# Optimization experiments

Measured on AMD Instinct MI355X. Metric: run time of the kernel, lower is better.

Reference implementation:

```python
import jax, jax.numpy as jnp
import numpy as np

H, DH = 4, 64          # heads, dim_head (match init_kwargs)
E = 128                # edge_dim
INNER = H * DH
NEG = -jnp.finfo(jnp.float32).max


def setup_inputs() -> dict:
    key = jax.random.key(0)
    ks = jax.random.split(key, 8)
    b, i, j = 1, 256, 256
    s = lambda fan_in: 1.0 / np.sqrt(fan_in)
    return {
        "inter_edges": jax.random.normal(ks[0], (b, i, j, E), jnp.float32),
        "ab_mask": jnp.ones((b, i), dtype=bool),
        "at_mask": jnp.ones((b, j), dtype=bool),
        "Wq": jax.random.normal(ks[1], (E, INNER), jnp.float32) * s(E),
        "Wk": jax.random.normal(ks[2], (E, INNER), jnp.float32) * s(E),
        "Wv": jax.random.normal(ks[3], (E, INNER), jnp.float32) * s(E),
        "Web": jax.random.normal(ks[4], (E, H), jnp.float32) * s(E),
        "Wg": jax.random.normal(ks[5], (E, INNER), jnp.float32) * s(E),
        "bg": jnp.zeros((INNER,), jnp.float32),
        "Wo": jax.random.normal(ks[6], (INNER, E), jnp.float32) * s(INNER),
        "bo": jnp.zeros((E,), jnp.float32),
    }


def reference(inter_edges, ab_mask, at_mask, Wq, Wk, Wv, Web, Wg, bg, Wo, bo):
    b, i, j, e = inter_edges.shape  # b must be 1 (bias broadcast in original)

    def split_hd(t):  # 'b i j (h d) -> (b h) i j d'
        return t.reshape(b, i, j, H, DH).transpose(0, 3, 1, 2, 4).reshape(b * H, i, j, DH)

    q = split_hd(inter_edges @ Wq)
    k = split_hd(inter_edges @ Wk)
    v = split_hd(inter_edges @ Wv)

    # to_ebias: [b,i,j,h].transpose(0,-1) -> [h,i,j,b]; broadcasts over key axis (b==1)
    z_bias = jnp.swapaxes(inter_edges @ Web, 0, -1)

    # gate uses (d h) split order, unlike q/k/v's (h d)
    gate = jax.nn.sigmoid(inter_edges @ Wg + bg)
    z_gate = gate.reshape(b, i, j, DH, H).transpose(0, 4, 1, 2, 3).reshape(b * H, i, j, DH)

    sim = jnp.einsum('hijd,hikd->hijk', q, k) * (DH ** -0.5) + z_bias

    mask = ab_mask[:, :, None] & at_mask[:, None, :]          # [b,i,j]
    mask = jnp.repeat(mask, H, axis=0)                        # [(b h),i,j]
    sim = jnp.where(mask[..., None], sim, NEG)                # mask whole (i,j) query rows

    attn = jax.nn.softmax(sim, axis=-1)
    # original einsum 'h i j k, h i j d -> h i j d' == v * attn.sum(-1)
    out = v * jnp.sum(attn, axis=-1, keepdims=True)
    out = z_gate * out
    out = out.reshape(b, H, i, j, DH).transpose(0, 2, 3, 1, 4).reshape(b, i, j, INNER)
    return out @ Wo + bo
```

## Files before the change

### kernel.cpp

```cpp
#include <hip/hip_runtime.h>

typedef __attribute__((ext_vector_type(8))) short short8;
typedef __attribute__((ext_vector_type(4))) float f32x4;

__device__ __forceinline__ unsigned short f2b(float x) {
  union { float f; unsigned u; } v; v.f = x;
  unsigned r = v.u + 0x7fffu + ((v.u >> 16) & 1u);
  return (unsigned short)(r >> 16);
}

__global__ __launch_bounds__(256) void prep_kernel(
    const float* __restrict__ Wv, const float* __restrict__ Wg,
    const float* __restrict__ bgv, const float* __restrict__ Wo,
    unsigned short* __restrict__ W1T, unsigned short* __restrict__ WoT,
    float* __restrict__ bg2)
{
  int t = blockIdx.x * 256 + threadIdx.x;
  if (t < 512 * 128) {
    int c = t >> 7, e = t & 127;
    float val;
    if (c < 256) {
      val = Wv[e * 256 + c];
    } else {
      int cc = c - 256;
      val = Wg[e * 256 + ((cc & 63) << 2) + (cc >> 6)];
    }
    W1T[t] = f2b(val);
  } else if (t < 512 * 128 + 128 * 256) {
    int u = t - 512 * 128;
    int o = u >> 8, c = u & 255;
    WoT[u] = f2b(Wo[c * 128 + o]);
  } else if (t < 512 * 128 + 128 * 256 + 256) {
    int c = t - (512 * 128 + 128 * 256);
    bg2[c] = bgv[((c & 63) << 2) + (c >> 6)];
  }
}

__global__ __launch_bounds__(256) void fused_kernel(
    const float* __restrict__ X,
    const unsigned short* __restrict__ W1T,
    const unsigned short* __restrict__ WoT,
    const float* __restrict__ bg2,
    const float* __restrict__ bo,
    float* __restrict__ Out)
{
  __shared__ unsigned short Xs[64 * 128];
  __shared__ unsigned short Ys[64 * 256];

  const int tid  = threadIdx.x;
  const int lane = tid & 63;
  const int wave = tid >> 6;
  const int l15  = lane & 15;
  const int lhi  = lane >> 4;
  const long rowbase = (long)blockIdx.x * 64;

  const float4* Xblk = reinterpret_cast<const float4*>(X + rowbase * 128);
  #pragma unroll
  for (int it = 0; it < 8; ++it) {
    int idx4 = it * 256 + tid;
    float4 f = Xblk[idx4];
    int e0  = idx4 * 4;
    int row = e0 >> 7;
    int col = e0 & 127;
    int sidx = (row * 128 + col) ^ ((row & 7) << 3);
    ushort4 u;
    u.x = f2b(f.x); u.y = f2b(f.y); u.z = f2b(f.z); u.w = f2b(f.w);
    *reinterpret_cast<ushort4*>(&Xs[sidx]) = u;
  }
  __syncthreads();

  short8 afrag[4][4];
  #pragma unroll
  for (int mt = 0; mt < 4; ++mt) {
    int row = mt * 16 + l15;
    #pragma unroll
    for (int ks = 0; ks < 4; ++ks) {
      int sidx = (row * 128 + ks * 32 + lhi * 8) ^ ((row & 7) << 3);
      afrag[mt][ks] = *reinterpret_cast<const short8*>(&Xs[sidx]);
    }
  }

  const f32x4 vzero = {0.f, 0.f, 0.f, 0.f};

  #pragma unroll
  for (int t = 0; t < 4; ++t) {
    int c0 = (wave * 4 + t) * 16;
    const unsigned short* WVrow = W1T + (c0 + l15) * 128 + lhi * 8;
    const unsigned short* WGrow = WVrow + 256 * 128;
    f32x4 accV[4], accG[4];
    #pragma unroll
    for (int mt = 0; mt < 4; ++mt) { accV[mt] = vzero; accG[mt] = vzero; }
    #pragma unroll
    for (int ks = 0; ks < 4; ++ks) {
      short8 bV = *reinterpret_cast<const short8*>(WVrow + ks * 32);
      short8 bG = *reinterpret_cast<const short8*>(WGrow + ks * 32);
      #pragma unroll
      for (int mt = 0; mt < 4; ++mt) {
        accV[mt] = __builtin_amdgcn_mfma_f32_16x16x32_bf16(afrag[mt][ks], bV, accV[mt], 0, 0, 0);
        accG[mt] = __builtin_amdgcn_mfma_f32_16x16x32_bf16(afrag[mt][ks], bG, accG[mt], 0, 0, 0);
      }
    }
    float bgval = bg2[c0 + l15];
    #pragma unroll
    for (int mt = 0; mt < 4; ++mt) {
      #pragma unroll
      for (int r = 0; r < 4; ++r) {
        int row = mt * 16 + lhi * 4 + r;
        float z = accG[mt][r] + bgval;
        float g = 1.0f / (1.0f + __expf(-z));
        float y = g * accV[mt][r];
        int sidx = (row * 256 + c0 + l15) ^ ((row & 7) << 3);
        Ys[sidx] = f2b(y);
      }
    }
  }
  __syncthreads();

  f32x4 acc2[2][4];
  #pragma unroll
  for (int nn = 0; nn < 2; ++nn)
    #pragma unroll
    for (int mt = 0; mt < 4; ++mt) acc2[nn][mt] = vzero;

  int o0 = wave * 16;
  #pragma unroll
  for (int ks = 0; ks < 8; ++ks) {
    short8 b0 = *reinterpret_cast<const short8*>(WoT + (o0 + l15) * 256 + ks * 32 + lhi * 8);
    short8 b1 = *reinterpret_cast<const short8*>(WoT + (64 + o0 + l15) * 256 + ks * 32 + lhi * 8);
    #pragma unroll
    for (int mt = 0; mt < 4; ++mt) {
      int row = mt * 16 + l15;
      int sidx = (row * 256 + ks * 32 + lhi * 8) ^ ((row & 7) << 3);
      short8 a = *reinterpret_cast<const short8*>(&Ys[sidx]);
      acc2[0][mt] = __builtin_amdgcn_mfma_f32_16x16x32_bf16(a, b0, acc2[0][mt], 0, 0, 0);
      acc2[1][mt] = __builtin_amdgcn_mfma_f32_16x16x32_bf16(a, b1, acc2[1][mt], 0, 0, 0);
    }
  }
  #pragma unroll
  for (int nn = 0; nn < 2; ++nn) {
    int o = nn * 64 + o0 + l15;
    float bov = bo[o];
    #pragma unroll
    for (int mt = 0; mt < 4; ++mt) {
      #pragma unroll
      for (int r = 0; r < 4; ++r) {
        long row = rowbase + mt * 16 + lhi * 4 + r;
        Out[row * 128 + o] = acc2[nn][mt][r] + bov;
      }
    }
  }
}

extern "C" void kernel_launch(void* const* d_in, const int* in_sizes, int n_in,
                              void* d_out, int out_size, void* d_ws, size_t ws_size,
                              hipStream_t stream) {
  const float* X   = (const float*)d_in[0];
  const float* Wv  = (const float*)d_in[5];
  const float* Wg  = (const float*)d_in[7];
  const float* bg  = (const float*)d_in[8];
  const float* Wo  = (const float*)d_in[9];
  const float* bo  = (const float*)d_in[10];

  unsigned short* W1T = (unsigned short*)d_ws;
  unsigned short* WoT = W1T + 512 * 128;
  float*          bg2 = (float*)(WoT + 128 * 256);

  prep_kernel<<<385, 256, 0, stream>>>(Wv, Wg, bg, Wo, W1T, WoT, bg2);

  float* Out = (float*)d_out;
  fused_kernel<<<1024, 256, 0, stream>>>(X, W1T, WoT, bg2, bo, Out);
}
```

Before: 126.3 us.

## Alias X and Y LDS buffers, raise occupancy hint, coalesce prep reads

The fused kernel now reuses a single shared-memory buffer for both the bf16 input tile and the gated intermediate, with an extra barrier after the A fragments are loaded into registers. This cuts LDS per block from 48KB to 32KB, and the launch bound now asks for 5 waves per SIMD so more blocks can be resident. The prep kernel is rewritten to read the weights in coalesced order and scatter the transposed writes. The tighter register budget could cause spills, and the extra barrier adds a sync.

```diff
diff --git a/kernel.cpp b/kernel.cpp
--- a/kernel.cpp
+++ b/kernel.cpp
@@ -16,27 +16,25 @@
     float* __restrict__ bg2)
 {
   int t = blockIdx.x * 256 + threadIdx.x;
-  if (t < 512 * 128) {
-    int c = t >> 7, e = t & 127;
-    float val;
-    if (c < 256) {
-      val = Wv[e * 256 + c];
-    } else {
-      int cc = c - 256;
-      val = Wg[e * 256 + ((cc & 63) << 2) + (cc >> 6)];
-    }
-    W1T[t] = f2b(val);
-  } else if (t < 512 * 128 + 128 * 256) {
-    int u = t - 512 * 128;
-    int o = u >> 8, c = u & 255;
-    WoT[u] = f2b(Wo[c * 128 + o]);
-  } else if (t < 512 * 128 + 128 * 256 + 256) {
-    int c = t - (512 * 128 + 128 * 256);
-    bg2[c] = bgv[((c & 63) << 2) + (c >> 6)];
+  if (t < 32768) {
+    int e = t >> 8, c = t & 255;
+    W1T[c * 128 + e] = f2b(Wv[t]);
+  } else if (t < 65536) {
+    int s = t - 32768;
+    int e = s >> 8, g = s & 255;
+    int cc = ((g & 3) << 6) + (g >> 2);
+    W1T[(256 + cc) * 128 + e] = f2b(Wg[s]);
+  } else if (t < 65536 + 32768) {
+    int s = t - 65536;
+    int c = s >> 7, o = s & 127;
+    WoT[o * 256 + c] = f2b(Wo[s]);
+  } else if (t < 65536 + 32768 + 256) {
+    int g = t - (65536 + 32768);
+    bg2[((g & 3) << 6) + (g >> 2)] = bgv[g];
   }
 }
 
-__global__ __launch_bounds__(256) void fused_kernel(
+__global__ __launch_bounds__(256, 5) void fused_kernel(
     const float* __restrict__ X,
     const unsigned short* __restrict__ W1T,
     const unsigned short* __restrict__ WoT,
@@ -44,8 +42,9 @@
     const float* __restrict__ bo,
     float* __restrict__ Out)
 {
-  __shared__ unsigned short Xs[64 * 128];
-  __shared__ unsigned short Ys[64 * 256];
+  __shared__ unsigned short smem[64 * 256];
+  unsigned short* Xs = smem;
+  unsigned short* Ys = smem;
 
   const int tid  = threadIdx.x;
   const int lane = tid & 63;
@@ -79,6 +78,7 @@
       afrag[mt][ks] = *reinterpret_cast<const short8*>(&Xs[sidx]);
     }
   }
+  __syncthreads();
 
   const f32x4 vzero = {0.f, 0.f, 0.f, 0.f};
 
@@ -165,7 +165,8 @@
   unsigned short* WoT = W1T + 512 * 128;
   float*          bg2 = (float*)(WoT + 128 * 256);
 
-  prep_kernel<<<385, 256, 0, stream>>>(Wv, Wg, bg, Wo, W1T, WoT, bg2);
+  prep_kernel<<<(65536 + 32768 + 256 + 255) / 256 + 1, 256, 0, stream>>>(
+      Wv, Wg, bg, Wo, W1T, WoT, bg2);
 
   float* Out = (float*)d_out;
   fused_kernel<<<1024, 256, 0, stream>>>(X, W1T, WoT, bg2, bo, Out);
```

Result: slower. 164.2 us (+30.0%).
